# Performance work log

Hardware: AMD Instinct MI355X
Metric: run time of the kernel (lower is better)

The kernel has to match this reference:

```python
import jax, jax.numpy as jnp
import numpy as np

B, N, DIM = 32, 3136, 64
H, DH, AGENTS = 8, 8, 49
INNER = H * DH  # 64
SCALE = DH ** -0.5


def setup_inputs() -> dict:
    key = jax.random.key(0)
    ks = jax.random.split(key, 7)
    s = 0.05
    return {
        "x1": jax.random.normal(ks[0], (B, N, DIM), jnp.float32),
        "x2": jax.random.normal(ks[1], (B, N, INNER), jnp.float32),
        "Wq": jax.random.normal(ks[2], (INNER, DIM), jnp.float32) * s,   # to_q (out,in)
        "Wk": jax.random.normal(ks[3], (DIM, INNER), jnp.float32) * s,   # to_k
        "Wv": jax.random.normal(ks[4], (DIM, INNER), jnp.float32) * s,   # to_v
        "Wo": jax.random.normal(ks[5], (2 * DIM, 2 * DIM), jnp.float32) * s,  # to_out linear
        "bo": jax.random.normal(ks[6], (2 * DIM,), jnp.float32) * s,
    }


def _split_heads(t):
    # (b, n, h*d) -> (b, h, n, d)
    b, n, hd = t.shape
    return t.reshape(b, n, H, hd // H).transpose(0, 2, 1, 3)


def reference(x1, x2, Wq, Wk, Wv, Wo, bo):
    b, n, _ = x1.shape
    q = x1 @ Wq.T                      # (b, n, 64)
    k = x2 @ Wk.T                      # (b, n, dim=64)
    v = x2 @ Wv.T
    # AdaptiveAvgPool2d((49, dim)): n % 49 == 0 and channel 64->64 is identity,
    # so pooling is an exact block mean over the sequence axis.
    agent = q.reshape(b, AGENTS, n // AGENTS, q.shape[-1]).mean(axis=2)  # (b, 49, 64)

    agent_h = _split_heads(agent)      # (b, h, 49, d)
    q1 = _split_heads(q)               # (b, h, n, d)
    k_h = _split_heads(k)
    v_h = _split_heads(v)

    # stage 0: agent tokens attend over keys/values (dropout is identity at eval)
    dots0 = jnp.einsum('bhid,bhjd->bhij', agent_h, k_h) * SCALE   # (b,h,49,n)
    attn0 = jax.nn.softmax(dots0, axis=-1)
    out0 = jnp.einsum('bhij,bhjd->bhid', attn0, v_h)              # (b,h,49,d)

    # stage 1: queries attend over agent tokens
    dots1 = jnp.einsum('bhid,bhjd->bhij', q1, agent_h) * SCALE    # (b,h,n,49)
    attn1 = jax.nn.softmax(dots1, axis=-1)
    out1 = jnp.einsum('bhij,bhjd->bhid', attn1, out0)             # (b,h,n,d)

    out1 = out1.transpose(0, 2, 1, 3).reshape(b, n, -1)           # (b,n,64)
    out1 = jnp.concatenate([out1, x1], axis=-1)                   # (b,n,128)
    return out1 @ Wo.T + bo
```

## Files before the change

kernel.cpp:

```cpp
#include <hip/hip_runtime.h>
#include <hip/hip_bf16.h>

#define NB 32
#define NSEQ 3136
#define NDIM 64
#define NH 8
#define NAG 49
#define SPLIT 4

static constexpr float kScale = 0.35355339059327378f;
static constexpr float kLog2e = 1.4426950408889634f;

typedef unsigned short us;
typedef __attribute__((ext_vector_type(8))) __bf16 bf16x8;
typedef __attribute__((ext_vector_type(4))) __bf16 bf16x4;
typedef __attribute__((ext_vector_type(2))) _Float16 f16x2;
typedef __attribute__((ext_vector_type(4))) _Float16 f16x4;
typedef __attribute__((ext_vector_type(8))) _Float16 f16x8;
typedef __attribute__((ext_vector_type(4))) float f32x4;
typedef __attribute__((ext_vector_type(2))) float f32x2;

__device__ __forceinline__ f32x2 up2(unsigned int u) {
  return (f32x2){__uint_as_float(u << 16), __uint_as_float(u & 0xffff0000u)};
}

__device__ __forceinline__ float fexp2(float x) {
#if __has_builtin(__builtin_amdgcn_exp2f)
  return __builtin_amdgcn_exp2f(x);
#else
  return exp2f(x);
#endif
}

__device__ __forceinline__ float frcp(float x) {
#if __has_builtin(__builtin_amdgcn_rcpf)
  return __builtin_amdgcn_rcpf(x);
#else
  return 1.f / x;
#endif
}

__device__ __forceinline__ unsigned pk2(float a, float b) {
#if __has_builtin(__builtin_amdgcn_cvt_pkrtz)
  return __builtin_bit_cast(unsigned, __builtin_amdgcn_cvt_pkrtz(a, b));
#else
  f16x2 v = {(_Float16)a, (_Float16)b};
  return __builtin_bit_cast(unsigned, v);
#endif
}

__global__ __launch_bounds__(256) void prep_kernel(
    const float* __restrict__ Wq, const float* __restrict__ Wk,
    const float* __restrict__ Wv, const float* __restrict__ Wo,
    __bf16* __restrict__ wq, __bf16* __restrict__ wk, __bf16* __restrict__ wv,
    __bf16* __restrict__ wo, us* __restrict__ kvhk, us* __restrict__ vt) {
  int i = blockIdx.x * 256 + threadIdx.x;
  wo[i] = (__bf16)Wo[i];
  if (i < 4096) { wq[i] = (__bf16)Wq[i]; wk[i] = (__bf16)Wk[i]; wv[i] = (__bf16)Wv[i]; }
  if (i < 32) kvhk[(size_t)NB * NH * NSEQ * 8 + i] = 0;
  const us one = 0x3C00;
  for (size_t j = i; j < (size_t)NB * NH * NSEQ; j += 16384) {
    size_t bh = j / NSEQ, tok = j - bh * NSEQ;
    vt[(bh * 9 + 8) * NSEQ + tok] = one;
  }
}

__global__ __launch_bounds__(256, 4) void qkv_agent_kernel(
    const float* __restrict__ x1, const float* __restrict__ x2,
    const float* __restrict__ Wq, const __bf16* __restrict__ wk,
    const __bf16* __restrict__ wv, us* __restrict__ kvhk, us* __restrict__ vt,
    float* __restrict__ agent, us* __restrict__ agf16) {
  __shared__ __align__(16) __bf16 xb[64][72];
  __shared__ __align__(16) float red[4][64];
  __shared__ __align__(16) float marr[64];
  const int a = blockIdx.x, b = blockIdx.y, t = threadIdx.x;
  const int i64 = t & 63, cb = t >> 6;
  const int w = cb, lr = (t >> 4) & 3, lc = t & 15;

  bf16x8 ak0 = *(const bf16x8*)(wk + (size_t)(w * 16 + lc) * NDIM + lr * 8);
  bf16x8 ak1 = *(const bf16x8*)(wk + (size_t)(w * 16 + lc) * NDIM + 32 + lr * 8);
  bf16x8 av0 = *(const bf16x8*)(wv + (size_t)(w * 16 + lc) * NDIM + lr * 8);
  bf16x8 av1 = *(const bf16x8*)(wv + (size_t)(w * 16 + lc) * NDIM + 32 + lr * 8);

  {
    const float4* s2 = (const float4*)(x2 + ((size_t)(b * NSEQ) + a * 64 + i64) * NDIM + cb * 16);
    float4 v0 = s2[0], v1 = s2[1], v2 = s2[2], v3 = s2[3];
    bf16x8 p0, p1;
    p0[0]=(__bf16)v0.x; p0[1]=(__bf16)v0.y; p0[2]=(__bf16)v0.z; p0[3]=(__bf16)v0.w;
    p0[4]=(__bf16)v1.x; p0[5]=(__bf16)v1.y; p0[6]=(__bf16)v1.z; p0[7]=(__bf16)v1.w;
    p1[0]=(__bf16)v2.x; p1[1]=(__bf16)v2.y; p1[2]=(__bf16)v2.z; p1[3]=(__bf16)v2.w;
    p1[4]=(__bf16)v3.x; p1[5]=(__bf16)v3.y; p1[6]=(__bf16)v3.z; p1[7]=(__bf16)v3.w;
    *(bf16x8*)&xb[i64][cb * 16] = p0; *(bf16x8*)&xb[i64][cb * 16 + 8] = p1;
  }
  {
    const float* xc = x1 + ((size_t)(b * NSEQ) + a * 64 + cb * 16) * NDIM + i64;
    float cs = 0.f;
#pragma unroll
    for (int i = 0; i < 16; ++i) cs += xc[i * NDIM];
    red[cb][i64] = cs;
  }
  __syncthreads();

  f32x4 acck[4], accv[4];
#pragma unroll
  for (int i = 0; i < 4; ++i) {
    acck[i] = (f32x4){0.f, 0.f, 0.f, 0.f};
    accv[i] = (f32x4){0.f, 0.f, 0.f, 0.f};
  }
#pragma unroll
  for (int nt = 0; nt < 4; ++nt) {
    bf16x8 x0 = *(const bf16x8*)&xb[nt * 16 + lc][lr * 8];
    bf16x8 x1f = *(const bf16x8*)&xb[nt * 16 + lc][32 + lr * 8];
    acck[nt] = __builtin_amdgcn_mfma_f32_16x16x32_bf16(ak0, x0, acck[nt], 0, 0, 0);
    acck[nt] = __builtin_amdgcn_mfma_f32_16x16x32_bf16(ak1, x1f, acck[nt], 0, 0, 0);
    accv[nt] = __builtin_amdgcn_mfma_f32_16x16x32_bf16(av0, x0, accv[nt], 0, 0, 0);
    accv[nt] = __builtin_amdgcn_mfma_f32_16x16x32_bf16(av1, x1f, accv[nt], 0, 0, 0);
  }
  const int head = 2 * w + (lr >> 1), sb = (lr & 1) * 4;
  {
    _Float16* kdst = (_Float16*)kvhk + ((size_t)(b * NH + head) * NSEQ) * 8 + sb;
    _Float16* vtb = (_Float16*)vt + ((size_t)(b * NH + head) * 9) * NSEQ;
#pragma unroll
    for (int nt = 0; nt < 4; ++nt) {
      const int tok = a * 64 + nt * 16 + lc;
      f16x4 pk4;
      pk4[0]=(_Float16)acck[nt][0]; pk4[1]=(_Float16)acck[nt][1];
      pk4[2]=(_Float16)acck[nt][2]; pk4[3]=(_Float16)acck[nt][3];
      *(f16x4*)(kdst + (size_t)tok * 8) = pk4;
#pragma unroll
      for (int j = 0; j < 4; ++j)
        vtb[(size_t)(sb + j) * NSEQ + tok] = (_Float16)accv[nt][j];
    }
  }

  if (t < 64) marr[t] = red[0][t] + red[1][t] + red[2][t] + red[3][t];
  __syncthreads();
  if (t < 64) {
    const float4* wqr = (const float4*)(Wq + (size_t)t * NDIM);
    const float4* mm = (const float4*)marr;
    float s0 = 0.f;
#pragma unroll
    for (int i = 0; i < 16; ++i) {
      float4 wv4 = wqr[i], m4 = mm[i];
      s0 += wv4.x * m4.x + wv4.y * m4.y + wv4.z * m4.z + wv4.w * m4.w;
    }
    const float val = s0 * (kScale * kLog2e / 64.f);
    const size_t idx = (((size_t)b * NH + (t >> 3)) * NAG + a) * 8 + (t & 7);
    agent[idx] = val;
    ((_Float16*)agf16)[idx] = (_Float16)val;
  }
}

__global__ __launch_bounds__(256, 4) void stage0_kernel(
    const us* __restrict__ kvhk, const us* __restrict__ vt,
    const us* __restrict__ agf16, float* __restrict__ pvs_z) {
  __shared__ _Float16 pshuf[4][4][16][40];
  __shared__ float redS[64][12];
  const int h = blockIdx.x, b = blockIdx.y, z = blockIdx.z;
  const int t = threadIdx.x, l = t & 63, w = t >> 6;
  for (int i = t; i < 64 * 12; i += 256) (&redS[0][0])[i] = 0.f;

  const int lg = l >> 4, lm = l & 15;
  const size_t bh = (size_t)b * NH + h;
  const us* kb = kvhk + bh * ((size_t)NSEQ * 8);
  const us* vb = vt + bh * ((size_t)9 * NSEQ);
  const us* ab = agf16 + bh * (NAG * 8);

  f16x8 ba[4];
#pragma unroll
  for (int at = 0; at < 4; ++at) {
    f16x8 v = (f16x8)(_Float16)0.0f;
    if (lg == 0) {
      int row = at * 16 + lm; if (row > 48) row = 48;
      v = *(const f16x8*)(ab + row * 8);
    }
    ba[at] = v;
  }
  const us* vrow = vb + (size_t)((lm > 8) ? 8 : lm) * NSEQ + lg * 8;

  f32x4 accPV[4];
#pragma unroll
  for (int i = 0; i < 4; ++i) accPV[i] = (f32x4){0.f, 0.f, 0.f, 0.f};

  _Float16* ps = &pshuf[w][0][0][0];
  const int iw = z * 4 + w;
  __syncthreads();

  for (int c = iw; c < 98; c += SPLIT * 4) {
    f16x8 aK0 = *(const f16x8*)(kb + ((size_t)c * 32 + lm) * 8 + lg * 8);
    f16x8 aK1 = *(const f16x8*)(kb + ((size_t)c * 32 + 16 + lm) * 8 + lg * 8);
    f16x8 bV = *(const f16x8*)(vrow + c * 32);
#pragma unroll
    for (int at = 0; at < 4; ++at) {
      f32x4 s0 = __builtin_amdgcn_mfma_f32_16x16x32_f16(
          aK0, ba[at], (f32x4){0.f, 0.f, 0.f, 0.f}, 0, 0, 0);
      f32x4 s1 = __builtin_amdgcn_mfma_f32_16x16x32_f16(
          aK1, ba[at], (f32x4){0.f, 0.f, 0.f, 0.f}, 0, 0, 0);
      unsigned p00 = pk2(fexp2(s0[0]), fexp2(s0[1]));
      unsigned p01 = pk2(fexp2(s0[2]), fexp2(s0[3]));
      unsigned p10 = pk2(fexp2(s1[0]), fexp2(s1[1]));
      unsigned p11 = pk2(fexp2(s1[2]), fexp2(s1[3]));
      unsigned long long q0 = ((unsigned long long)p01 << 32) | p00;
      unsigned long long q1 = ((unsigned long long)p11 << 32) | p10;
      _Float16* prow = ps + (size_t)(at * 16 + lm) * 40;
      *(unsigned long long*)(prow + lg * 4) = q0;
      *(unsigned long long*)(prow + 16 + lg * 4) = q1;
    }
#pragma unroll
    for (int at = 0; at < 4; ++at) {
      f16x8 aP = *(const f16x8*)(ps + (size_t)(at * 16 + lm) * 40 + lg * 8);
      accPV[at] = __builtin_amdgcn_mfma_f32_16x16x32_f16(aP, bV, accPV[at], 0, 0, 0);
    }
  }

  if (lm < 9) {
#pragma unroll
    for (int at = 0; at < 4; ++at)
#pragma unroll
      for (int jj = 0; jj < 4; ++jj) {
        const int ag = at * 16 + lg * 4 + jj;
        if (ag < NAG) atomicAdd(&redS[ag][lm], accPV[at][jj]);
      }
  }
  __syncthreads();
  float* pz = pvs_z + ((size_t)z * (NB * NH) + bh) * (NAG * 12);
  for (int i = t; i < NAG * 9; i += 256) {
    pz[(i / 9) * 12 + (i % 9)] = redS[i / 9][i % 9];
  }
}

__global__ __launch_bounds__(512, 6) void stage1_out_kernel(
    const float* __restrict__ x1, const __bf16* __restrict__ wq,
    const float* __restrict__ agent, const float* __restrict__ pvs_z,
    const __bf16* __restrict__ wo, const float* __restrict__ bo,
    float* __restrict__ out) {
  __shared__ __align__(16) __bf16 xa[64][72];
  __shared__ __align__(16) __bf16 qcat[64][72];
  __shared__ __align__(16) float aot[392 * 20];
  const int tile = blockIdx.x, b = blockIdx.y;
  const int t = threadIdx.x, tokl = t & 63, h = t >> 6;
  const int w = h, lr = (t >> 4) & 3, lc = t & 15;
  const int mtile = w & 3, thalf = w >> 2;

  bf16x8 wqf0 = *(const bf16x8*)(wq + (size_t)(mtile * 16 + lc) * NDIM + lr * 8);
  bf16x8 wqf1 = *(const bf16x8*)(wq + (size_t)(mtile * 16 + lc) * NDIM + 32 + lr * 8);
  bf16x8 wof[4];
#pragma unroll
  for (int ks = 0; ks < 4; ++ks)
    wof[ks] = *(const bf16x8*)(wo + (size_t)(w * 16 + lc) * 128 + ks * 32 + lr * 8);
  f32x4 bv = *(const f32x4*)(bo + w * 16 + lr * 4);

  f32x4 ag0, ag1;
  f32x4 pvA = (f32x4){0.f,0.f,0.f,0.f}, pvB = (f32x4){0.f,0.f,0.f,0.f};
  float sden = 0.f;
  if (t < NH * NAG) {
    const int hi2 = t / NAG, ai = t - hi2 * NAG;
    const float* ap = agent + (((size_t)b * NH + hi2) * NAG + ai) * 8;
    ag0 = *(const f32x4*)ap; ag1 = *(const f32x4*)(ap + 4);
#pragma unroll
    for (int zz = 0; zz < SPLIT; ++zz) {
      const float* pp = pvs_z +
          (((size_t)zz * (NB * NH) + (size_t)b * NH + hi2) * NAG + ai) * 12;
      pvA += *(const f32x4*)pp;
      pvB += *(const f32x4*)(pp + 4);
      sden += pp[8];
    }
  }

  {
    const float4* src = (const float4*)(x1 + ((size_t)b * NSEQ + tile * 64 + tokl) * NDIM + h * 8);
    float4 v0 = src[0], v1 = src[1];
    bf16x8 p;
    p[0]=(__bf16)v0.x; p[1]=(__bf16)v0.y; p[2]=(__bf16)v0.z; p[3]=(__bf16)v0.w;
    p[4]=(__bf16)v1.x; p[5]=(__bf16)v1.y; p[6]=(__bf16)v1.z; p[7]=(__bf16)v1.w;
    *(bf16x8*)&xa[tokl][h * 8] = p;
  }
  __syncthreads();

  {
    f32x4 aq[2];
    aq[0] = (f32x4){0.f,0.f,0.f,0.f}; aq[1] = (f32x4){0.f,0.f,0.f,0.f};
#pragma unroll
    for (int nt = 0; nt < 2; ++nt) {
      bf16x8 bx0 = *(const bf16x8*)&xa[thalf * 32 + nt * 16 + lc][lr * 8];
      bf16x8 bx1 = *(const bf16x8*)&xa[thalf * 32 + nt * 16 + lc][32 + lr * 8];
      aq[nt] = __builtin_amdgcn_mfma_f32_16x16x32_bf16(wqf0, bx0, aq[nt], 0, 0, 0);
      aq[nt] = __builtin_amdgcn_mfma_f32_16x16x32_bf16(wqf1, bx1, aq[nt], 0, 0, 0);
    }
#pragma unroll
    for (int nt = 0; nt < 2; ++nt) {
      bf16x4 pk;
      pk[0]=(__bf16)aq[nt][0]; pk[1]=(__bf16)aq[nt][1];
      pk[2]=(__bf16)aq[nt][2]; pk[3]=(__bf16)aq[nt][3];
      *(bf16x4*)&qcat[thalf * 32 + nt * 16 + lc][mtile * 16 + lr * 4] = pk;
    }
  }
  if (t < NH * NAG) {
    float inv = frcp(sden);
    float* dst = aot + t * 20;
    *(f32x4*)dst = ag0;
    *(f32x4*)(dst + 4) = ag1;
    *(f32x4*)(dst + 8)  = pvA * inv;
    *(f32x4*)(dst + 12) = pvB * inv;
  }
  __syncthreads();

  {
    uint4 qv = *(const uint4*)&qcat[tokl][h * 8];
    f32x2 q01 = up2(qv.x), q23 = up2(qv.y), q45 = up2(qv.z), q67 = up2(qv.w);
    const float* hrow = aot + h * (NAG * 20);
    float s = 0.f;
    f32x2 o01 = {0.f,0.f}, o23 = {0.f,0.f}, o45 = {0.f,0.f}, o67 = {0.f,0.f};
#pragma unroll 7
    for (int a2 = 0; a2 < NAG; ++a2) {
      const float* r = hrow + a2 * 20;
      f32x4 A0 = *(const f32x4*)r,        A1 = *(const f32x4*)(r + 4);
      f32x4 P0 = *(const f32x4*)(r + 8),  P1 = *(const f32x4*)(r + 12);
      f32x2 d = q01 * (f32x2){A0[0], A0[1]};
      d += q23 * (f32x2){A0[2], A0[3]};
      d += q45 * (f32x2){A1[0], A1[1]};
      d += q67 * (f32x2){A1[2], A1[3]};
      float p = fexp2(d[0] + d[1]);
      s += p;
      f32x2 pp = {p, p};
      o01 += pp * (f32x2){P0[0], P0[1]}; o23 += pp * (f32x2){P0[2], P0[3]};
      o45 += pp * (f32x2){P1[0], P1[1]}; o67 += pp * (f32x2){P1[2], P1[3]};
    }
    float inv = frcp(s);
    bf16x8 pc;
    pc[0]=(__bf16)(o01[0]*inv); pc[1]=(__bf16)(o01[1]*inv);
    pc[2]=(__bf16)(o23[0]*inv); pc[3]=(__bf16)(o23[1]*inv);
    pc[4]=(__bf16)(o45[0]*inv); pc[5]=(__bf16)(o45[1]*inv);
    pc[6]=(__bf16)(o67[0]*inv); pc[7]=(__bf16)(o67[1]*inv);
    *(bf16x8*)&qcat[tokl][h * 8] = pc;
  }
  __syncthreads();

  {
    f32x4 acc[4];
#pragma unroll
    for (int i = 0; i < 4; ++i) acc[i] = (f32x4){0.f,0.f,0.f,0.f};
#pragma unroll
    for (int ks = 0; ks < 4; ++ks) {
#pragma unroll
      for (int nt = 0; nt < 4; ++nt) {
        bf16x8 bx = (ks < 2) ? *(const bf16x8*)&qcat[nt * 16 + lc][ks * 32 + lr * 8]
                             : *(const bf16x8*)&xa[nt * 16 + lc][(ks - 2) * 32 + lr * 8];
        acc[nt] = __builtin_amdgcn_mfma_f32_16x16x32_bf16(wof[ks], bx, acc[nt], 0, 0, 0);
      }
    }
#pragma unroll
    for (int nt = 0; nt < 4; ++nt) {
      f32x4 v = acc[nt] + bv;
      float* dst = out + ((size_t)b * NSEQ + tile * 64 + nt * 16 + lc) * 128 + w * 16 + lr * 4;
      *(f32x4*)dst = v;
    }
  }
}

extern "C" void kernel_launch(void* const* d_in, const int* in_sizes, int n_in,
                              void* d_out, int out_size, void* d_ws, size_t ws_size,
                              hipStream_t stream) {
  (void)in_sizes; (void)n_in; (void)out_size; (void)ws_size;
  const float* x1 = (const float*)d_in[0];
  const float* x2 = (const float*)d_in[1];
  const float* Wq = (const float*)d_in[2];
  const float* Wk = (const float*)d_in[3];
  const float* Wv = (const float*)d_in[4];
  const float* Wo = (const float*)d_in[5];
  const float* bo = (const float*)d_in[6];
  float* out = (float*)d_out;

  us* vt = (us*)d_ws;
  us* kvhk = vt + (size_t)NB * NH * 9 * NSEQ;
  float* agent = (float*)(kvhk + (size_t)NB * NH * NSEQ * 8 + 32);
  us* agf16 = (us*)(agent + (size_t)NB * NH * NAG * 8);
  float* pvs_z = (float*)(agf16 + (size_t)NB * NH * NAG * 8);
  __bf16* wq_bf = (__bf16*)(pvs_z + (size_t)SPLIT * NB * NH * NAG * 12);
  __bf16* wk_bf = wq_bf + 4096;
  __bf16* wv_bf = wk_bf + 4096;
  __bf16* wo_bf = wv_bf + 4096;

  prep_kernel<<<dim3(64), 256, 0, stream>>>(Wq, Wk, Wv, Wo, wq_bf, wk_bf, wv_bf,
                                            wo_bf, kvhk, vt);
  qkv_agent_kernel<<<dim3(NAG, NB), 256, 0, stream>>>(x1, x2, Wq, wk_bf, wv_bf,
                                                      kvhk, vt, agent, agf16);
  stage0_kernel<<<dim3(NH, NB, SPLIT), 256, 0, stream>>>(kvhk, vt, agf16, pvs_z);
  stage1_out_kernel<<<dim3(NAG, NB), 512, 0, stream>>>(x1, wq_bf, agent, pvs_z,
                                                       wo_bf, bo, out);
}
```

Measured before the change: 86.26 us.

## Stage V transpose through LDS, prefetch stage0 loads, precombine agent outputs in fp16

The qkv kernel now transposes V in shared memory and writes it as coalesced 16-byte rows instead of scattered 2-byte stores. The stage0 loop software-prefetches the next K/V chunk. A new small kernel reduces the split partial sums once per (batch, head) into a packed fp16 agent/output table. The stage1 kernel loads that table, runs its inner attention loop in fp16 with fdot2 and packed fp16 FMAs, and defers the Wo fragment loads to cut register pressure (launch bound raised to 8). This adds a launch and lowers the precision of the stage1 accumulation.

```diff
diff --git a/kernel.cpp b/kernel.cpp
--- a/kernel.cpp
+++ b/kernel.cpp
@@ -13,16 +13,11 @@
 
 typedef unsigned short us;
 typedef __attribute__((ext_vector_type(8))) __bf16 bf16x8;
-typedef __attribute__((ext_vector_type(4))) __bf16 bf16x4;
 typedef __attribute__((ext_vector_type(2))) _Float16 f16x2;
 typedef __attribute__((ext_vector_type(4))) _Float16 f16x4;
 typedef __attribute__((ext_vector_type(8))) _Float16 f16x8;
 typedef __attribute__((ext_vector_type(4))) float f32x4;
 typedef __attribute__((ext_vector_type(2))) float f32x2;
-
-__device__ __forceinline__ f32x2 up2(unsigned int u) {
-  return (f32x2){__uint_as_float(u << 16), __uint_as_float(u & 0xffff0000u)};
-}
 
 __device__ __forceinline__ float fexp2(float x) {
 #if __has_builtin(__builtin_amdgcn_exp2f)
@@ -48,6 +43,8 @@
   return __builtin_bit_cast(unsigned, v);
 #endif
 }
+
+__device__ __forceinline__ f16x2 bch(unsigned u) { return __builtin_bit_cast(f16x2, u); }
 
 __global__ __launch_bounds__(256) void prep_kernel(
     const float* __restrict__ Wq, const float* __restrict__ Wk,
@@ -69,7 +66,7 @@
     const float* __restrict__ x1, const float* __restrict__ x2,
     const float* __restrict__ Wq, const __bf16* __restrict__ wk,
     const __bf16* __restrict__ wv, us* __restrict__ kvhk, us* __restrict__ vt,
-    float* __restrict__ agent, us* __restrict__ agf16) {
+    us* __restrict__ agf16) {
   __shared__ __align__(16) __bf16 xb[64][72];
   __shared__ __align__(16) float red[4][64];
   __shared__ __align__(16) float marr[64];
@@ -119,7 +116,6 @@
   const int head = 2 * w + (lr >> 1), sb = (lr & 1) * 4;
   {
     _Float16* kdst = (_Float16*)kvhk + ((size_t)(b * NH + head) * NSEQ) * 8 + sb;
-    _Float16* vtb = (_Float16*)vt + ((size_t)(b * NH + head) * 9) * NSEQ;
 #pragma unroll
     for (int nt = 0; nt < 4; ++nt) {
       const int tok = a * 64 + nt * 16 + lc;
@@ -127,14 +123,32 @@
       pk4[0]=(_Float16)acck[nt][0]; pk4[1]=(_Float16)acck[nt][1];
       pk4[2]=(_Float16)acck[nt][2]; pk4[3]=(_Float16)acck[nt][3];
       *(f16x4*)(kdst + (size_t)tok * 8) = pk4;
-#pragma unroll
-      for (int j = 0; j < 4; ++j)
-        vtb[(size_t)(sb + j) * NSEQ + tok] = (_Float16)accv[nt][j];
-    }
-  }
-
+    }
+  }
+  __syncthreads();
+
+  _Float16 (*vtile)[72] = (_Float16(*)[72])xb;
+  {
+    const int f0 = w * 16 + lr * 4;
+#pragma unroll
+    for (int nt = 0; nt < 4; ++nt) {
+      const int tok = nt * 16 + lc;
+#pragma unroll
+      for (int j = 0; j < 4; ++j) vtile[f0 + j][tok] = (_Float16)accv[nt][j];
+    }
+  }
   if (t < 64) marr[t] = red[0][t] + red[1][t] + red[2][t] + red[3][t];
   __syncthreads();
+
+  {
+    const int r = t >> 2, p = t & 3;
+    _Float16* drow = (_Float16*)vt +
+        ((size_t)(b * NH + (r >> 3)) * 9 + (r & 7)) * NSEQ + a * 64 + p * 16;
+    f16x8 v0 = *(const f16x8*)&vtile[r][p * 16];
+    f16x8 v1 = *(const f16x8*)&vtile[r][p * 16 + 8];
+    *(f16x8*)drow = v0;
+    *(f16x8*)(drow + 8) = v1;
+  }
   if (t < 64) {
     const float4* wqr = (const float4*)(Wq + (size_t)t * NDIM);
     const float4* mm = (const float4*)marr;
@@ -145,9 +159,8 @@
       s0 += wv4.x * m4.x + wv4.y * m4.y + wv4.z * m4.z + wv4.w * m4.w;
     }
     const float val = s0 * (kScale * kLog2e / 64.f);
-    const size_t idx = (((size_t)b * NH + (t >> 3)) * NAG + a) * 8 + (t & 7);
-    agent[idx] = val;
-    ((_Float16*)agf16)[idx] = (_Float16)val;
+    ((_Float16*)agf16)[(((size_t)b * NH + (t >> 3)) * NAG + a) * 8 + (t & 7)] =
+        (_Float16)val;
   }
 }
 
@@ -186,10 +199,19 @@
   const int iw = z * 4 + w;
   __syncthreads();
 
-  for (int c = iw; c < 98; c += SPLIT * 4) {
-    f16x8 aK0 = *(const f16x8*)(kb + ((size_t)c * 32 + lm) * 8 + lg * 8);
-    f16x8 aK1 = *(const f16x8*)(kb + ((size_t)c * 32 + 16 + lm) * 8 + lg * 8);
-    f16x8 bV = *(const f16x8*)(vrow + c * 32);
+  f16x8 aK0, aK1, bV;
+  aK0 = *(const f16x8*)(kb + ((size_t)iw * 32 + lm) * 8 + lg * 8);
+  aK1 = *(const f16x8*)(kb + ((size_t)iw * 32 + 16 + lm) * 8 + lg * 8);
+  bV  = *(const f16x8*)(vrow + iw * 32);
+
+  for (int c = iw; c < 98; c += 16) {
+    f16x8 nK0, nK1, nV;
+    const int cn = c + 16;
+    if (cn < 98) {
+      nK0 = *(const f16x8*)(kb + ((size_t)cn * 32 + lm) * 8 + lg * 8);
+      nK1 = *(const f16x8*)(kb + ((size_t)cn * 32 + 16 + lm) * 8 + lg * 8);
+      nV  = *(const f16x8*)(vrow + cn * 32);
+    }
 #pragma unroll
     for (int at = 0; at < 4; ++at) {
       f32x4 s0 = __builtin_amdgcn_mfma_f32_16x16x32_f16(
@@ -211,6 +233,7 @@
       f16x8 aP = *(const f16x8*)(ps + (size_t)(at * 16 + lm) * 40 + lg * 8);
       accPV[at] = __builtin_amdgcn_mfma_f32_16x16x32_f16(aP, bV, accPV[at], 0, 0, 0);
     }
+    aK0 = nK0; aK1 = nK1; bV = nV;
   }
 
   if (lm < 9) {
@@ -229,14 +252,39 @@
   }
 }
 
-__global__ __launch_bounds__(512, 6) void stage1_out_kernel(
+__global__ __launch_bounds__(64) void aofin_kernel(
+    const us* __restrict__ agf16, const float* __restrict__ pvs_z,
+    us* __restrict__ aof16) {
+  const int h = blockIdx.x, b = blockIdx.y, t = threadIdx.x;
+  if (t >= NAG) return;
+  const size_t bh = (size_t)b * NH + h;
+  f32x4 pv0 = (f32x4){0.f,0.f,0.f,0.f}, pv1 = (f32x4){0.f,0.f,0.f,0.f};
+  float den = 0.f;
+#pragma unroll
+  for (int zz = 0; zz < SPLIT; ++zz) {
+    const float* pp = pvs_z + (((size_t)zz * (NB * NH) + bh) * NAG + t) * 12;
+    pv0 += *(const f32x4*)pp;
+    pv1 += *(const f32x4*)(pp + 4);
+    den += pp[8];
+  }
+  float inv = frcp(den);
+  pv0 *= inv; pv1 *= inv;
+  us* dst = aof16 + (bh * NAG + t) * 16;
+  *(uint4*)dst = *(const uint4*)(agf16 + (bh * NAG + t) * 8);
+  f16x4 a, c;
+  a[0]=(_Float16)pv0[0]; a[1]=(_Float16)pv0[1]; a[2]=(_Float16)pv0[2]; a[3]=(_Float16)pv0[3];
+  c[0]=(_Float16)pv1[0]; c[1]=(_Float16)pv1[1]; c[2]=(_Float16)pv1[2]; c[3]=(_Float16)pv1[3];
+  *(f16x4*)(dst + 8) = a;
+  *(f16x4*)(dst + 12) = c;
+}
+
+__global__ __launch_bounds__(512, 8) void stage1_out_kernel(
     const float* __restrict__ x1, const __bf16* __restrict__ wq,
-    const float* __restrict__ agent, const float* __restrict__ pvs_z,
-    const __bf16* __restrict__ wo, const float* __restrict__ bo,
-    float* __restrict__ out) {
+    const us* __restrict__ aof16, const __bf16* __restrict__ wo,
+    const float* __restrict__ bo, float* __restrict__ out) {
   __shared__ __align__(16) __bf16 xa[64][72];
-  __shared__ __align__(16) __bf16 qcat[64][72];
-  __shared__ __align__(16) float aot[392 * 20];
+  __shared__ __align__(16) us qcat[64][72];
+  __shared__ __align__(16) us aof[392 * 16];
   const int tile = blockIdx.x, b = blockIdx.y;
   const int t = threadIdx.x, tokl = t & 63, h = t >> 6;
   const int w = h, lr = (t >> 4) & 3, lc = t & 15;
@@ -244,28 +292,6 @@
 
   bf16x8 wqf0 = *(const bf16x8*)(wq + (size_t)(mtile * 16 + lc) * NDIM + lr * 8);
   bf16x8 wqf1 = *(const bf16x8*)(wq + (size_t)(mtile * 16 + lc) * NDIM + 32 + lr * 8);
-  bf16x8 wof[4];
-#pragma unroll
-  for (int ks = 0; ks < 4; ++ks)
-    wof[ks] = *(const bf16x8*)(wo + (size_t)(w * 16 + lc) * 128 + ks * 32 + lr * 8);
-  f32x4 bv = *(const f32x4*)(bo + w * 16 + lr * 4);
-
-  f32x4 ag0, ag1;
-  f32x4 pvA = (f32x4){0.f,0.f,0.f,0.f}, pvB = (f32x4){0.f,0.f,0.f,0.f};
-  float sden = 0.f;
-  if (t < NH * NAG) {
-    const int hi2 = t / NAG, ai = t - hi2 * NAG;
-    const float* ap = agent + (((size_t)b * NH + hi2) * NAG + ai) * 8;
-    ag0 = *(const f32x4*)ap; ag1 = *(const f32x4*)(ap + 4);
-#pragma unroll
-    for (int zz = 0; zz < SPLIT; ++zz) {
-      const float* pp = pvs_z +
-          (((size_t)zz * (NB * NH) + (size_t)b * NH + hi2) * NAG + ai) * 12;
-      pvA += *(const f32x4*)pp;
-      pvB += *(const f32x4*)(pp + 4);
-      sden += pp[8];
-    }
-  }
 
   {
     const float4* src = (const float4*)(x1 + ((size_t)b * NSEQ + tile * 64 + tokl) * NDIM + h * 8);
@@ -275,6 +301,11 @@
     p[4]=(__bf16)v1.x; p[5]=(__bf16)v1.y; p[6]=(__bf16)v1.z; p[7]=(__bf16)v1.w;
     *(bf16x8*)&xa[tokl][h * 8] = p;
   }
+  {
+    const uint4* src = (const uint4*)(aof16 + (size_t)b * (NH * NAG * 16));
+    uint4* dst = (uint4*)aof;
+    for (int i = t; i < 784; i += 512) dst[i] = src[i];
+  }
   __syncthreads();
 
   {
@@ -289,51 +320,58 @@
     }
 #pragma unroll
     for (int nt = 0; nt < 2; ++nt) {
-      bf16x4 pk;
-      pk[0]=(__bf16)aq[nt][0]; pk[1]=(__bf16)aq[nt][1];
-      pk[2]=(__bf16)aq[nt][2]; pk[3]=(__bf16)aq[nt][3];
-      *(bf16x4*)&qcat[thalf * 32 + nt * 16 + lc][mtile * 16 + lr * 4] = pk;
-    }
-  }
-  if (t < NH * NAG) {
-    float inv = frcp(sden);
-    float* dst = aot + t * 20;
-    *(f32x4*)dst = ag0;
-    *(f32x4*)(dst + 4) = ag1;
-    *(f32x4*)(dst + 8)  = pvA * inv;
-    *(f32x4*)(dst + 12) = pvB * inv;
+      f16x4 pk;
+      pk[0]=(_Float16)aq[nt][0]; pk[1]=(_Float16)aq[nt][1];
+      pk[2]=(_Float16)aq[nt][2]; pk[3]=(_Float16)aq[nt][3];
+      *(f16x4*)&qcat[thalf * 32 + nt * 16 + lc][mtile * 16 + lr * 4] = pk;
+    }
   }
   __syncthreads();
 
   {
     uint4 qv = *(const uint4*)&qcat[tokl][h * 8];
-    f32x2 q01 = up2(qv.x), q23 = up2(qv.y), q45 = up2(qv.z), q67 = up2(qv.w);
-    const float* hrow = aot + h * (NAG * 20);
+    f16x2 q0 = bch(qv.x), q1 = bch(qv.y), q2 = bch(qv.z), q3 = bch(qv.w);
+    const us* hrow = aof + (h * NAG) * 16;
     float s = 0.f;
-    f32x2 o01 = {0.f,0.f}, o23 = {0.f,0.f}, o45 = {0.f,0.f}, o67 = {0.f,0.f};
+    f16x2 o01 = (f16x2)(_Float16)0.f, o23 = o01, o45 = o01, o67 = o01;
 #pragma unroll 7
     for (int a2 = 0; a2 < NAG; ++a2) {
-      const float* r = hrow + a2 * 20;
-      f32x4 A0 = *(const f32x4*)r,        A1 = *(const f32x4*)(r + 4);
-      f32x4 P0 = *(const f32x4*)(r + 8),  P1 = *(const f32x4*)(r + 12);
-      f32x2 d = q01 * (f32x2){A0[0], A0[1]};
-      d += q23 * (f32x2){A0[2], A0[3]};
-      d += q45 * (f32x2){A1[0], A1[1]};
-      d += q67 * (f32x2){A1[2], A1[3]};
-      float p = fexp2(d[0] + d[1]);
+      const us* r = hrow + a2 * 16;
+      uint4 A = *(const uint4*)r;
+      uint4 V = *(const uint4*)(r + 8);
+      float lg;
+#if __has_builtin(__builtin_amdgcn_fdot2)
+      lg = __builtin_amdgcn_fdot2(q0, bch(A.x), 0.f, false);
+      lg = __builtin_amdgcn_fdot2(q1, bch(A.y), lg, false);
+      lg = __builtin_amdgcn_fdot2(q2, bch(A.z), lg, false);
+      lg = __builtin_amdgcn_fdot2(q3, bch(A.w), lg, false);
+#else
+      f16x2 a0 = bch(A.x), a1 = bch(A.y), a2_ = bch(A.z), a3 = bch(A.w);
+      lg = (float)q0[0]*(float)a0[0] + (float)q0[1]*(float)a0[1]
+         + (float)q1[0]*(float)a1[0] + (float)q1[1]*(float)a1[1]
+         + (float)q2[0]*(float)a2_[0] + (float)q2[1]*(float)a2_[1]
+         + (float)q3[0]*(float)a3[0] + (float)q3[1]*(float)a3[1];
+#endif
+      float p = fexp2(lg);
       s += p;
-      f32x2 pp = {p, p};
-      o01 += pp * (f32x2){P0[0], P0[1]}; o23 += pp * (f32x2){P0[2], P0[3]};
-      o45 += pp * (f32x2){P1[0], P1[1]}; o67 += pp * (f32x2){P1[2], P1[3]};
+      _Float16 pf = (_Float16)p;
+      f16x2 pp = {pf, pf};
+      o01 += pp * bch(V.x); o23 += pp * bch(V.y);
+      o45 += pp * bch(V.z); o67 += pp * bch(V.w);
     }
     float inv = frcp(s);
     bf16x8 pc;
-    pc[0]=(__bf16)(o01[0]*inv); pc[1]=(__bf16)(o01[1]*inv);
-    pc[2]=(__bf16)(o23[0]*inv); pc[3]=(__bf16)(o23[1]*inv);
-    pc[4]=(__bf16)(o45[0]*inv); pc[5]=(__bf16)(o45[1]*inv);
-    pc[6]=(__bf16)(o67[0]*inv); pc[7]=(__bf16)(o67[1]*inv);
+    pc[0]=(__bf16)((float)o01[0]*inv); pc[1]=(__bf16)((float)o01[1]*inv);
+    pc[2]=(__bf16)((float)o23[0]*inv); pc[3]=(__bf16)((float)o23[1]*inv);
+    pc[4]=(__bf16)((float)o45[0]*inv); pc[5]=(__bf16)((float)o45[1]*inv);
+    pc[6]=(__bf16)((float)o67[0]*inv); pc[7]=(__bf16)((float)o67[1]*inv);
     *(bf16x8*)&qcat[tokl][h * 8] = pc;
   }
+  bf16x8 wof[4];
+#pragma unroll
+  for (int ks = 0; ks < 4; ++ks)
+    wof[ks] = *(const bf16x8*)(wo + (size_t)(w * 16 + lc) * 128 + ks * 32 + lr * 8);
+  f32x4 bv = *(const f32x4*)(bo + w * 16 + lr * 4);
   __syncthreads();
 
   {
@@ -373,10 +411,10 @@
 
   us* vt = (us*)d_ws;
   us* kvhk = vt + (size_t)NB * NH * 9 * NSEQ;
-  float* agent = (float*)(kvhk + (size_t)NB * NH * NSEQ * 8 + 32);
-  us* agf16 = (us*)(agent + (size_t)NB * NH * NAG * 8);
+  us* agf16 = kvhk + (size_t)NB * NH * NSEQ * 8 + 32;
   float* pvs_z = (float*)(agf16 + (size_t)NB * NH * NAG * 8);
-  __bf16* wq_bf = (__bf16*)(pvs_z + (size_t)SPLIT * NB * NH * NAG * 12);
+  us* aof16 = (us*)(pvs_z + (size_t)SPLIT * NB * NH * NAG * 12);
+  __bf16* wq_bf = (__bf16*)(aof16 + (size_t)NB * NH * NAG * 16);
   __bf16* wk_bf = wq_bf + 4096;
   __bf16* wv_bf = wk_bf + 4096;
   __bf16* wo_bf = wv_bf + 4096;
@@ -384,8 +422,9 @@
   prep_kernel<<<dim3(64), 256, 0, stream>>>(Wq, Wk, Wv, Wo, wq_bf, wk_bf, wv_bf,
                                             wo_bf, kvhk, vt);
   qkv_agent_kernel<<<dim3(NAG, NB), 256, 0, stream>>>(x1, x2, Wq, wk_bf, wv_bf,
-                                                      kvhk, vt, agent, agf16);
+                                                      kvhk, vt, agf16);
   stage0_kernel<<<dim3(NH, NB, SPLIT), 256, 0, stream>>>(kvhk, vt, agf16, pvs_z);
-  stage1_out_kernel<<<dim3(NAG, NB), 512, 0, stream>>>(x1, wq_bf, agent, pvs_z,
-                                                       wo_bf, bo, out);
-}
+  aofin_kernel<<<dim3(NH, NB), 64, 0, stream>>>(agf16, pvs_z, aof16);
+  stage1_out_kernel<<<dim3(NAG, NB), 512, 0, stream>>>(x1, wq_bf, aof16, wo_bf,
+                                                       bo, out);
+}
```

Result: faster. 79.69 us (-7.6%).
